# Kernel tuning notes

Measured on AMD Instinct MI355X. Metric: run time of the kernel, lower is better.

Reference implementation:

```python
import jax, jax.numpy as jnp
import numpy as np

B, T, V, E, U = 64, 128, 20000, 512, 1024


def _gru_dir(x_tbe, W, Uw, bi, bh):
    """Keras GRU (reset_after=True, gate order z,r,h). x_tbe: [T,B,E]."""
    # Precompute all input projections in one big GEMM: [T,B,3U]
    xg = jnp.einsum('tbe,eg->tbg', x_tbe, W) + bi

    def step(h, xg_t):
        hg = h @ Uw + bh                       # [B,3U]
        xz, xr, xh = jnp.split(xg_t, 3, axis=-1)
        hz, hr, hh = jnp.split(hg, 3, axis=-1)
        z = jax.nn.sigmoid(xz + hz)            # update gate
        r = jax.nn.sigmoid(xr + hr)            # reset gate
        hcand = jnp.tanh(xh + r * hh)          # reset_after=True form
        h_new = z * h + (1.0 - z) * hcand
        return h_new, h_new

    h0 = jnp.zeros((x_tbe.shape[1], Uw.shape[0]), x_tbe.dtype)
    hT, outs = jax.lax.scan(step, h0, xg)      # outs: [T,B,U]
    return outs, hT


def setup_inputs() -> dict:
    key = jax.random.key(0)
    ks = jax.random.split(key, 8)
    s_in = 1.0 / np.sqrt(E)
    s_rec = 1.0 / np.sqrt(U)
    return {
        'tokens': jax.random.randint(ks[0], (B, T), 0, V),
        'emb': jax.random.normal(ks[1], (V, E), jnp.float32) * 0.05,
        'Wf': jax.random.normal(ks[2], (E, 3 * U), jnp.float32) * s_in,
        'Uf': jax.random.normal(ks[3], (U, 3 * U), jnp.float32) * s_rec,
        'bif': jnp.zeros((3 * U,), jnp.float32),
        'bhf': jnp.zeros((3 * U,), jnp.float32),
        'Wb': jax.random.normal(ks[4], (E, 3 * U), jnp.float32) * s_in,
        'Ub': jax.random.normal(ks[5], (U, 3 * U), jnp.float32) * s_rec,
        'bib': jnp.zeros((3 * U,), jnp.float32),
        'bhb': jnp.zeros((3 * U,), jnp.float32),
    }


def reference(tokens, emb, Wf, Uf, bif, bhf, Wb, Ub, bib, bhb):
    tokens = tokens[:, ::-1]                    # tf.reverse(inputs, [-1])
    x = emb[tokens]                             # embedding lookup -> [B,T,E]
    x_t = jnp.swapaxes(x, 0, 1)                 # [T,B,E]
    out_f, h_f = _gru_dir(x_t, Wf, Uf, bif, bhf)
    out_b, h_b = _gru_dir(x_t[::-1], Wb, Ub, bib, bhb)
    out_b = out_b[::-1]                         # re-align backward outputs
    outputs = jnp.swapaxes(out_f + out_b, 0, 1)  # merge_mode='sum' -> [B,T,U]
    hidden = jnp.concatenate([h_f, h_b], axis=1)  # [B,2U]
    return outputs, hidden
```

## Files before the change

kernel.cpp:

```cpp
#include <hip/hip_runtime.h>
#include <hip/hip_bf16.h>

typedef float f32;
typedef __hip_bfloat16 bf16;
typedef unsigned int u32;
typedef unsigned short u16;

#define T_LEN 128
#define B_SZ  64
#define E_DIM 512
#define U_DIM 1024
#define G3    3072
#define BTU   (B_SZ * T_LEN * U_DIM)

typedef __attribute__((ext_vector_type(8))) __bf16 bf16x8;
typedef __attribute__((ext_vector_type(8))) u16  us8;
typedef __attribute__((ext_vector_type(4))) u16  us4;
typedef __attribute__((ext_vector_type(4))) f32  f32x4;

union F8 { us8 u; bf16x8 b; };

#define WS_USW 0u
#define WS_HQ  25165824u
#define WS_XG  26214400u

#define STEP_LDS 106496
#define XG_LDS   66048

__device__ __forceinline__ u32 f32_to_bf16_rne(f32 x) {
  u32 b = __float_as_uint(x);
  return (b + 0x7fffu + ((b >> 16) & 1u)) >> 16;
}

__global__ __launch_bounds__(256) void transpose_split(
    const f32* __restrict__ Uf, const f32* __restrict__ Ub, u16* __restrict__ USW)
{
  __shared__ f32 tile[32][33];
  const int d = blockIdx.z;
  const f32* Uw = d ? Ub : Uf;
  const int c0 = blockIdx.x * 32;
  const int k0 = blockIdx.y * 32;
  const int tx = threadIdx.x & 31;
  const int ty = threadIdx.x >> 5;
#pragma unroll
  for (int i = 0; i < 4; i++) {
    int kl = ty + i * 8;
    tile[kl][tx] = Uw[(size_t)(k0 + kl) * G3 + c0 + tx];
  }
  __syncthreads();
#pragma unroll
  for (int i = 0; i < 4; i++) {
    int cl = ty + i * 8;
    int c  = c0 + cl;
    f32 val = tile[tx][cl];
    int g = c >> 10, u = c & 1023;
    int blk = d * 128 + (u >> 3);
    int r   = g * 8 + (u & 7);
    u32 hib = f32_to_bf16_rne(val);
    f32 rem = val - __uint_as_float(hib << 16);
    u32 lob = f32_to_bf16_rne(rem);
    int k = k0 + tx;
    int slot = (k >> 3) ^ (r & 7);
    size_t base = ((size_t)blk * 2) * (24 * 1024);
    size_t off  = (size_t)r * 1024 + slot * 8 + (k & 7);
    USW[base + off] = (u16)hib;
    USW[base + (size_t)24 * 1024 + off] = (u16)lob;
  }
}

__global__ __launch_bounds__(256) void xg_gemm_mfma(
    const int* __restrict__ tokens, const f32* __restrict__ emb,
    const f32* __restrict__ Wf, const f32* __restrict__ bif,
    const f32* __restrict__ Wb, const f32* __restrict__ bib,
    bf16* __restrict__ XG)
{
  extern __shared__ u16 XL[];
  u16* Ash = XL;
  u16* Bsh = XL + 16384;
  int* tok_s = (int*)(XL + 32768);

  const int tid = threadIdx.x;
  const int n0 = blockIdx.x * 128;
  const int by = blockIdx.y;
  const int dir = by >> 6;
  const int s0 = (by & 63) * 2;
  const f32* W  = dir ? Wb : Wf;
  const f32* bi = dir ? bib : bif;

  if (tid < 128) {
    int srow = s0 + (tid >> 6);
    int b = tid & 63;
    int t_orig = dir ? srow : (T_LEN - 1 - srow);
    tok_s[tid] = tokens[b * T_LEN + t_orig];
  }
  __syncthreads();

  const int wv = tid >> 6;
  const int lane = tid & 63;
  const int arow = tid >> 1;
  const int akoff = (tid & 1) * 32;
  const int bcol = tid & 127;
  const int bkoff = (tid >> 7) * 32;

  f32x4 acc[2][8];
#pragma unroll
  for (int mi = 0; mi < 2; mi++)
#pragma unroll
    for (int ni = 0; ni < 8; ni++) acc[mi][ni] = (f32x4){0.f, 0.f, 0.f, 0.f};

  const f32* asrc0 = emb + (size_t)tok_s[arow] * E_DIM + akoff;

  for (int kk = 0; kk < 8; kk++) {
    __syncthreads();
    {
      const f32* src = asrc0 + kk * 64;
#pragma unroll
      for (int g = 0; g < 4; g++) {
        float4 v0 = *(const float4*)(src + g * 8);
        float4 v1 = *(const float4*)(src + g * 8 + 4);
        f32 vv[8] = {v0.x,v0.y,v0.z,v0.w,v1.x,v1.y,v1.z,v1.w};
        us8 h8, l8;
#pragma unroll
        for (int e = 0; e < 8; e++) {
          u32 bb = __float_as_uint(vv[e]);
          h8[e] = (u16)(bb >> 16);
          f32 rem = vv[e] - __uint_as_float(bb & 0xffff0000u);
          l8[e] = (u16)f32_to_bf16_rne(rem);
        }
        int sl = (((akoff >> 3) + g) ^ (arow & 7)) * 8;
        *(us8*)&Ash[(size_t)arow * 64 + sl] = h8;
        *(us8*)&Ash[(size_t)(128 + arow) * 64 + sl] = l8;
      }
    }
    {
      const f32* src = W + (size_t)(kk * 64 + bkoff) * G3 + n0 + bcol;
#pragma unroll
      for (int g = 0; g < 4; g++) {
        us8 h8, l8;
#pragma unroll
        for (int e = 0; e < 8; e++) {
          f32 v = src[(size_t)(g * 8 + e) * G3];
          u32 bb = __float_as_uint(v);
          h8[e] = (u16)(bb >> 16);
          f32 rem = v - __uint_as_float(bb & 0xffff0000u);
          l8[e] = (u16)f32_to_bf16_rne(rem);
        }
        int sl = (((bkoff >> 3) + g) ^ (bcol & 7)) * 8;
        *(us8*)&Bsh[(size_t)bcol * 64 + sl] = h8;
        *(us8*)&Bsh[(size_t)(128 + bcol) * 64 + sl] = l8;
      }
    }
    __syncthreads();
#pragma unroll
    for (int ks = 0; ks < 2; ks++) {
      F8 ah[2], al[2];
#pragma unroll
      for (int mi = 0; mi < 2; mi++) {
        int row = wv * 32 + mi * 16 + (lane & 15);
        int sl = ((ks * 4 + (lane >> 4)) ^ (row & 7)) * 8;
        ah[mi].u = *(const us8*)&Ash[(size_t)row * 64 + sl];
        al[mi].u = *(const us8*)&Ash[(size_t)(128 + row) * 64 + sl];
      }
#pragma unroll
      for (int ni = 0; ni < 8; ni++) {
        int col = ni * 16 + (lane & 15);
        int sl = ((ks * 4 + (lane >> 4)) ^ (col & 7)) * 8;
        F8 bh, bl;
        bh.u = *(const us8*)&Bsh[(size_t)col * 64 + sl];
        bl.u = *(const us8*)&Bsh[(size_t)(128 + col) * 64 + sl];
#pragma unroll
        for (int mi = 0; mi < 2; mi++) {
          acc[mi][ni] = __builtin_amdgcn_mfma_f32_16x16x32_bf16(ah[mi].b, bh.b, acc[mi][ni], 0, 0, 0);
          acc[mi][ni] = __builtin_amdgcn_mfma_f32_16x16x32_bf16(ah[mi].b, bl.b, acc[mi][ni], 0, 0, 0);
          acc[mi][ni] = __builtin_amdgcn_mfma_f32_16x16x32_bf16(al[mi].b, bh.b, acc[mi][ni], 0, 0, 0);
        }
      }
    }
  }
#pragma unroll
  for (int ni = 0; ni < 8; ni++) {
    int ncol = n0 + ni * 16 + (lane & 15);
    f32 bv = bi[ncol];
#pragma unroll
    for (int mi = 0; mi < 2; mi++) {
#pragma unroll
      for (int j = 0; j < 4; j++) {
        int row = wv * 32 + mi * 16 + (lane >> 4) * 4 + j;
        int srow = s0 + (row >> 6);
        int b = row & 63;
        XG[((size_t)(dir * T_LEN + srow) * B_SZ + b) * G3 + ncol] =
            __float2bfloat16(acc[mi][ni][j] + bv);
      }
    }
  }
}

__global__ __launch_bounds__(512) void gru_step4(
    const u16* __restrict__ USW,
    u16* __restrict__ Hq2,
    const u16* __restrict__ XG,
    const f32* __restrict__ bhf, const f32* __restrict__ bhb,
    f32* __restrict__ out, int s)
{
  extern __shared__ u16 Us[];
  const int blk = blockIdx.x;
  const int dir = blk >> 7;
  const int su  = (blk & 127) * 8;
  const int tid = threadIdx.x;
  const int lane = tid & 63;
  const int w  = tid >> 6;
  const int nw = w & 3, kw = w >> 2;

  const int bb = nw * 16 + (lane & 15);
  const int ko = (lane >> 4) * 8;
  const int kq = kw * 512;
  const int r0 = lane & 15;
  const int r1t = 16 + (lane & 15);
  const int r1 = r1t > 23 ? 23 : r1t;

  const int rb_h0 = (0 * 24 + r0) * 2048;
  const int rb_l0 = (1 * 24 + r0) * 2048;
  const int rb_h1 = (0 * 24 + r1) * 2048;
  const int rb_l1 = (1 * 24 + r1) * 2048;
  const int sw0 = r0 & 7, sw1 = r1 & 7;

  const int bufr = s & 1, bufw = bufr ^ 1;
  const u16* HrHi = Hq2 + (size_t)(((bufr * 2 + 0) * 2 + dir) * 64 + bb) * 1024;
  const u16* HrLo = Hq2 + (size_t)(((bufr * 2 + 1) * 2 + dir) * 64 + bb) * 1024;

  F8 h_hi0, h_lo0, h_hi1, h_lo1, h_hi2, h_lo2, h_hi3, h_lo3;
  if (s) {
    const u16* p = HrHi + kq + ko;
    const u16* q = HrLo + kq + ko;
    h_hi0.u = *(const us8*)(p);        h_lo0.u = *(const us8*)(q);
    h_hi1.u = *(const us8*)(p + 32);   h_lo1.u = *(const us8*)(q + 32);
    h_hi2.u = *(const us8*)(p + 64);   h_lo2.u = *(const us8*)(q + 64);
    h_hi3.u = *(const us8*)(p + 96);   h_lo3.u = *(const us8*)(q + 96);
  }

  {
    const us8* src = (const us8*)(USW + (size_t)blk * (2 * 24 * 1024));
    us8* dst = (us8*)Us;
#pragma unroll
    for (int i = 0; i < 12; i++) dst[tid + i * 512] = src[tid + i * 512];
  }

  __syncthreads();

  f32x4 acc0 = {0.f, 0.f, 0.f, 0.f};
  f32x4 acc1 = {0.f, 0.f, 0.f, 0.f};

#define DOMFMA(HHI, HLO, KS) { \
    const int slot = (kq >> 3) + (KS) * 4 + (lane >> 4); \
    F8 ah0, al0, ah1, al1; \
    ah0.u = *(const us8*)((const char*)Us + rb_h0 + ((slot ^ sw0) << 4)); \
    al0.u = *(const us8*)((const char*)Us + rb_l0 + ((slot ^ sw0) << 4)); \
    ah1.u = *(const us8*)((const char*)Us + rb_h1 + ((slot ^ sw1) << 4)); \
    al1.u = *(const us8*)((const char*)Us + rb_l1 + ((slot ^ sw1) << 4)); \
    acc0 = __builtin_amdgcn_mfma_f32_16x16x32_bf16(ah0.b, HHI.b, acc0, 0, 0, 0); \
    acc0 = __builtin_amdgcn_mfma_f32_16x16x32_bf16(ah0.b, HLO.b, acc0, 0, 0, 0); \
    acc0 = __builtin_amdgcn_mfma_f32_16x16x32_bf16(al0.b, HHI.b, acc0, 0, 0, 0); \
    acc1 = __builtin_amdgcn_mfma_f32_16x16x32_bf16(ah1.b, HHI.b, acc1, 0, 0, 0); \
    acc1 = __builtin_amdgcn_mfma_f32_16x16x32_bf16(ah1.b, HLO.b, acc1, 0, 0, 0); \
    acc1 = __builtin_amdgcn_mfma_f32_16x16x32_bf16(al1.b, HHI.b, acc1, 0, 0, 0); \
  }
#define LDH(HHI, HLO, KS) { \
    HHI.u = *(const us8*)(HrHi + kq + ko + (KS) * 32); \
    HLO.u = *(const us8*)(HrLo + kq + ko + (KS) * 32); \
  }

  if (s) {
    DOMFMA(h_hi0, h_lo0, 0)  LDH(h_hi0, h_lo0, 4)
    DOMFMA(h_hi1, h_lo1, 1)  LDH(h_hi1, h_lo1, 5)
    DOMFMA(h_hi2, h_lo2, 2)  LDH(h_hi2, h_lo2, 6)
    DOMFMA(h_hi3, h_lo3, 3)  LDH(h_hi3, h_lo3, 7)
    DOMFMA(h_hi0, h_lo0, 4)  LDH(h_hi0, h_lo0, 8)
    DOMFMA(h_hi1, h_lo1, 5)  LDH(h_hi1, h_lo1, 9)
    DOMFMA(h_hi2, h_lo2, 6)  LDH(h_hi2, h_lo2, 10)
    DOMFMA(h_hi3, h_lo3, 7)  LDH(h_hi3, h_lo3, 11)
    DOMFMA(h_hi0, h_lo0, 8)  LDH(h_hi0, h_lo0, 12)
    DOMFMA(h_hi1, h_lo1, 9)  LDH(h_hi1, h_lo1, 13)
    DOMFMA(h_hi2, h_lo2, 10) LDH(h_hi2, h_lo2, 14)
    DOMFMA(h_hi3, h_lo3, 11) LDH(h_hi3, h_lo3, 15)
    DOMFMA(h_hi0, h_lo0, 12)
    DOMFMA(h_hi1, h_lo1, 13)
    DOMFMA(h_hi2, h_lo2, 14)
    DOMFMA(h_hi3, h_lo3, 15)
  }
#undef DOMFMA
#undef LDH

  __syncthreads();
  f32* red = (f32*)(Us + 49152);
  if (kw == 1) {
    f32* p = red + (size_t)(nw * 64 + lane) * 8;
    *(f32x4*)p = acc0;
    *(f32x4*)(p + 4) = acc1;
  }
  __syncthreads();
  if (kw == 0) {
    const f32* p = red + (size_t)(nw * 64 + lane) * 8;
    f32x4 o0 = *(const f32x4*)p;
    f32x4 o1 = *(const f32x4*)(p + 4);
#pragma unroll
    for (int i = 0; i < 4; i++) { acc0[i] += o0[i]; acc1[i] += o1[i]; }

    f32 racc[4];
#pragma unroll
    for (int j = 0; j < 4; j++) racc[j] = __shfl_xor(acc0[j], 32);

    if (lane < 32) {
      const int ul0 = (lane >> 4) * 4;
      const int u0 = su + ul0;
      const u16* xgp = XG + ((size_t)(dir * T_LEN + s) * B_SZ + bb) * G3;
      us4 gz = *(const us4*)(xgp + u0 - su + su);
      gz = *(const us4*)(xgp + u0);
      us4 gr = *(const us4*)(xgp + 1024 + u0);
      us4 gh = *(const us4*)(xgp + 2048 + u0);
      us4 ohi = {0, 0, 0, 0}, olo = {0, 0, 0, 0};
      if (s) {
        ohi = *(const us4*)(HrHi + u0);
        olo = *(const us4*)(HrLo + u0);
      }
      const f32* bh = dir ? bhb : bhf;
      f32x4 hnv;
      us4 whi, wlo;
#pragma unroll
      for (int j = 0; j < 4; j++) {
        const int u = u0 + j;
        f32 hz = acc0[j] + bh[u];
        f32 hr = racc[j] + bh[1024 + u];
        f32 hh = acc1[j] + bh[2048 + u];
        f32 xz = __uint_as_float((u32)gz[j] << 16);
        f32 xr = __uint_as_float((u32)gr[j] << 16);
        f32 xh = __uint_as_float((u32)gh[j] << 16);
        f32 hold = __uint_as_float((u32)ohi[j] << 16) + __uint_as_float((u32)olo[j] << 16);

        f32 z  = 1.f / (1.f + expf(-(xz + hz)));
        f32 r  = 1.f / (1.f + expf(-(xr + hr)));
        f32 hc = tanhf(xh + r * hh);
        f32 hnew = z * hold + (1.f - z) * hc;

        u32 hib = f32_to_bf16_rne(hnew);
        f32 rem = hnew - __uint_as_float(hib << 16);
        u32 lob = f32_to_bf16_rne(rem);
        hnv[j] = hnew;
        whi[j] = (u16)hib;
        wlo[j] = (u16)lob;
      }
      u16* HwHi = Hq2 + (size_t)(((bufw * 2 + 0) * 2 + dir) * 64 + bb) * 1024;
      u16* HwLo = Hq2 + (size_t)(((bufw * 2 + 1) * 2 + dir) * 64 + bb) * 1024;
      *(us4*)(HwHi + u0) = whi;
      *(us4*)(HwLo + u0) = wlo;

      const int t = dir ? (T_LEN - 1 - s) : s;
      f32* op = out + ((size_t)bb * T_LEN + t) * U_DIM + u0;
      if (s < 64) {
        *(f32x4*)op = hnv;
      } else {
        f32x4 prev = *(const f32x4*)op;
#pragma unroll
        for (int j = 0; j < 4; j++) prev[j] += hnv[j];
        *(f32x4*)op = prev;
      }
      if (s == T_LEN - 1)
        *(f32x4*)(out + (size_t)BTU + (size_t)bb * 2048 + dir * 1024 + u0) = hnv;
    }
  }
}

extern "C" void kernel_launch(void* const* d_in, const int* in_sizes, int n_in,
                              void* d_out, int out_size, void* d_ws, size_t ws_size,
                              hipStream_t stream) {
  (void)in_sizes; (void)n_in; (void)out_size; (void)ws_size;
  const int* tokens = (const int*)d_in[0];
  const f32* emb = (const f32*)d_in[1];
  const f32* Wf  = (const f32*)d_in[2];
  const f32* Uf  = (const f32*)d_in[3];
  const f32* bif = (const f32*)d_in[4];
  const f32* bhf = (const f32*)d_in[5];
  const f32* Wb  = (const f32*)d_in[6];
  const f32* Ub  = (const f32*)d_in[7];
  const f32* bib = (const f32*)d_in[8];
  const f32* bhb = (const f32*)d_in[9];

  char* ws = (char*)d_ws;
  u16*  USW = (u16*)(ws + WS_USW);
  u16*  Hq2 = (u16*)(ws + WS_HQ);
  bf16* XG  = (bf16*)(ws + WS_XG);
  f32*  out = (f32*)d_out;

  transpose_split<<<dim3(96, 32, 2), 256, 0, stream>>>(Uf, Ub, USW);

  hipFuncSetAttribute((const void*)xg_gemm_mfma,
                      hipFuncAttributeMaxDynamicSharedMemorySize, XG_LDS);
  xg_gemm_mfma<<<dim3(24, 128), 256, XG_LDS, stream>>>(tokens, emb, Wf, bif, Wb, bib, XG);

  hipFuncSetAttribute((const void*)gru_step4,
                      hipFuncAttributeMaxDynamicSharedMemorySize, STEP_LDS);
  for (int s = 0; s < T_LEN; s++)
    gru_step4<<<256, 512, STEP_LDS, stream>>>(USW, Hq2, (const u16*)XG, bhf, bhb, out, s);
}
```

Baseline: 2.260 ms.

## Pack hidden-state hi/lo bf16 into u32 with unit-major layout, drop prefetch pipeline

New measurement: 1.892 ms. -16.3%, faster.

```diff
diff --git a/kernel.cpp b/kernel.cpp
--- a/kernel.cpp
+++ b/kernel.cpp
@@ -24,7 +24,7 @@
 #define WS_HQ  25165824u
 #define WS_XG  26214400u
 
-#define STEP_LDS 106496
+#define STEP_LDS 98304
 #define XG_LDS   66048
 
 __device__ __forceinline__ u32 f32_to_bf16_rne(f32 x) {
@@ -195,9 +195,9 @@
   }
 }
 
-__global__ __launch_bounds__(512) void gru_step4(
+__global__ __launch_bounds__(512) void gru_step5(
     const u16* __restrict__ USW,
-    u16* __restrict__ Hq2,
+    u32* __restrict__ Hq,
     const u16* __restrict__ XG,
     const f32* __restrict__ bhf, const f32* __restrict__ bhb,
     f32* __restrict__ out, int s)
@@ -211,9 +211,17 @@
   const int w  = tid >> 6;
   const int nw = w & 3, kw = w >> 2;
 
+  {
+    const us8* src = (const us8*)(USW + (size_t)blk * (2 * 24 * 1024));
+    us8* dst = (us8*)Us;
+    for (int i = tid; i < 6144; i += 512) dst[i] = src[i];
+  }
+
+  const u32* Hin  = Hq + (size_t)((s & 1) * 2 + dir) * (U_DIM * B_SZ);
+  u32*       Hout = Hq + (size_t)(((s + 1) & 1) * 2 + dir) * (U_DIM * B_SZ);
+
   const int bb = nw * 16 + (lane & 15);
   const int ko = (lane >> 4) * 8;
-  const int kq = kw * 512;
   const int r0 = lane & 15;
   const int r1t = 16 + (lane & 15);
   const int r1 = r1t > 23 ? 23 : r1t;
@@ -224,74 +232,42 @@
   const int rb_l1 = (1 * 24 + r1) * 2048;
   const int sw0 = r0 & 7, sw1 = r1 & 7;
 
-  const int bufr = s & 1, bufw = bufr ^ 1;
-  const u16* HrHi = Hq2 + (size_t)(((bufr * 2 + 0) * 2 + dir) * 64 + bb) * 1024;
-  const u16* HrLo = Hq2 + (size_t)(((bufr * 2 + 1) * 2 + dir) * 64 + bb) * 1024;
-
-  F8 h_hi0, h_lo0, h_hi1, h_lo1, h_hi2, h_lo2, h_hi3, h_lo3;
-  if (s) {
-    const u16* p = HrHi + kq + ko;
-    const u16* q = HrLo + kq + ko;
-    h_hi0.u = *(const us8*)(p);        h_lo0.u = *(const us8*)(q);
-    h_hi1.u = *(const us8*)(p + 32);   h_lo1.u = *(const us8*)(q + 32);
-    h_hi2.u = *(const us8*)(p + 64);   h_lo2.u = *(const us8*)(q + 64);
-    h_hi3.u = *(const us8*)(p + 96);   h_lo3.u = *(const us8*)(q + 96);
-  }
-
-  {
-    const us8* src = (const us8*)(USW + (size_t)blk * (2 * 24 * 1024));
-    us8* dst = (us8*)Us;
-#pragma unroll
-    for (int i = 0; i < 12; i++) dst[tid + i * 512] = src[tid + i * 512];
-  }
-
   __syncthreads();
 
   f32x4 acc0 = {0.f, 0.f, 0.f, 0.f};
   f32x4 acc1 = {0.f, 0.f, 0.f, 0.f};
 
-#define DOMFMA(HHI, HLO, KS) { \
-    const int slot = (kq >> 3) + (KS) * 4 + (lane >> 4); \
-    F8 ah0, al0, ah1, al1; \
-    ah0.u = *(const us8*)((const char*)Us + rb_h0 + ((slot ^ sw0) << 4)); \
-    al0.u = *(const us8*)((const char*)Us + rb_l0 + ((slot ^ sw0) << 4)); \
-    ah1.u = *(const us8*)((const char*)Us + rb_h1 + ((slot ^ sw1) << 4)); \
-    al1.u = *(const us8*)((const char*)Us + rb_l1 + ((slot ^ sw1) << 4)); \
-    acc0 = __builtin_amdgcn_mfma_f32_16x16x32_bf16(ah0.b, HHI.b, acc0, 0, 0, 0); \
-    acc0 = __builtin_amdgcn_mfma_f32_16x16x32_bf16(ah0.b, HLO.b, acc0, 0, 0, 0); \
-    acc0 = __builtin_amdgcn_mfma_f32_16x16x32_bf16(al0.b, HHI.b, acc0, 0, 0, 0); \
-    acc1 = __builtin_amdgcn_mfma_f32_16x16x32_bf16(ah1.b, HHI.b, acc1, 0, 0, 0); \
-    acc1 = __builtin_amdgcn_mfma_f32_16x16x32_bf16(ah1.b, HLO.b, acc1, 0, 0, 0); \
-    acc1 = __builtin_amdgcn_mfma_f32_16x16x32_bf16(al1.b, HHI.b, acc1, 0, 0, 0); \
-  }
-#define LDH(HHI, HLO, KS) { \
-    HHI.u = *(const us8*)(HrHi + kq + ko + (KS) * 32); \
-    HLO.u = *(const us8*)(HrLo + kq + ko + (KS) * 32); \
-  }
-
   if (s) {
-    DOMFMA(h_hi0, h_lo0, 0)  LDH(h_hi0, h_lo0, 4)
-    DOMFMA(h_hi1, h_lo1, 1)  LDH(h_hi1, h_lo1, 5)
-    DOMFMA(h_hi2, h_lo2, 2)  LDH(h_hi2, h_lo2, 6)
-    DOMFMA(h_hi3, h_lo3, 3)  LDH(h_hi3, h_lo3, 7)
-    DOMFMA(h_hi0, h_lo0, 4)  LDH(h_hi0, h_lo0, 8)
-    DOMFMA(h_hi1, h_lo1, 5)  LDH(h_hi1, h_lo1, 9)
-    DOMFMA(h_hi2, h_lo2, 6)  LDH(h_hi2, h_lo2, 10)
-    DOMFMA(h_hi3, h_lo3, 7)  LDH(h_hi3, h_lo3, 11)
-    DOMFMA(h_hi0, h_lo0, 8)  LDH(h_hi0, h_lo0, 12)
-    DOMFMA(h_hi1, h_lo1, 9)  LDH(h_hi1, h_lo1, 13)
-    DOMFMA(h_hi2, h_lo2, 10) LDH(h_hi2, h_lo2, 14)
-    DOMFMA(h_hi3, h_lo3, 11) LDH(h_hi3, h_lo3, 15)
-    DOMFMA(h_hi0, h_lo0, 12)
-    DOMFMA(h_hi1, h_lo1, 13)
-    DOMFMA(h_hi2, h_lo2, 14)
-    DOMFMA(h_hi3, h_lo3, 15)
-  }
-#undef DOMFMA
-#undef LDH
-
-  __syncthreads();
-  f32* red = (f32*)(Us + 49152);
+    for (int ks = 0; ks < 16; ks++) {
+      const int kb = kw * 512 + ks * 32;
+      const int slot = (kb >> 3) + (lane >> 4);
+      F8 ah0, al0, ah1, al1;
+      ah0.u = *(const us8*)((const char*)Us + rb_h0 + ((slot ^ sw0) << 4));
+      al0.u = *(const us8*)((const char*)Us + rb_l0 + ((slot ^ sw0) << 4));
+      ah1.u = *(const us8*)((const char*)Us + rb_h1 + ((slot ^ sw1) << 4));
+      al1.u = *(const us8*)((const char*)Us + rb_l1 + ((slot ^ sw1) << 4));
+
+      const int kbase = kb + ko;
+      u32 wd[8];
+#pragma unroll
+      for (int e = 0; e < 8; e++) wd[e] = Hin[(size_t)(kbase + e) * B_SZ + bb];
+      F8 bh_hi, bh_lo;
+#pragma unroll
+      for (int e = 0; e < 8; e++) {
+        bh_hi.u[e] = (u16)(wd[e] & 0xffffu);
+        bh_lo.u[e] = (u16)(wd[e] >> 16);
+      }
+      acc0 = __builtin_amdgcn_mfma_f32_16x16x32_bf16(ah0.b, bh_hi.b, acc0, 0, 0, 0);
+      acc0 = __builtin_amdgcn_mfma_f32_16x16x32_bf16(ah0.b, bh_lo.b, acc0, 0, 0, 0);
+      acc0 = __builtin_amdgcn_mfma_f32_16x16x32_bf16(al0.b, bh_hi.b, acc0, 0, 0, 0);
+      acc1 = __builtin_amdgcn_mfma_f32_16x16x32_bf16(ah1.b, bh_hi.b, acc1, 0, 0, 0);
+      acc1 = __builtin_amdgcn_mfma_f32_16x16x32_bf16(ah1.b, bh_lo.b, acc1, 0, 0, 0);
+      acc1 = __builtin_amdgcn_mfma_f32_16x16x32_bf16(al1.b, bh_hi.b, acc1, 0, 0, 0);
+    }
+  }
+
+  __syncthreads();
+  f32* red = (f32*)Us;
   if (kw == 1) {
     f32* p = red + (size_t)(nw * 64 + lane) * 8;
     *(f32x4*)p = acc0;
@@ -313,18 +289,11 @@
       const int ul0 = (lane >> 4) * 4;
       const int u0 = su + ul0;
       const u16* xgp = XG + ((size_t)(dir * T_LEN + s) * B_SZ + bb) * G3;
-      us4 gz = *(const us4*)(xgp + u0 - su + su);
-      gz = *(const us4*)(xgp + u0);
+      us4 gz = *(const us4*)(xgp + u0);
       us4 gr = *(const us4*)(xgp + 1024 + u0);
       us4 gh = *(const us4*)(xgp + 2048 + u0);
-      us4 ohi = {0, 0, 0, 0}, olo = {0, 0, 0, 0};
-      if (s) {
-        ohi = *(const us4*)(HrHi + u0);
-        olo = *(const us4*)(HrLo + u0);
-      }
       const f32* bh = dir ? bhb : bhf;
       f32x4 hnv;
-      us4 whi, wlo;
 #pragma unroll
       for (int j = 0; j < 4; j++) {
         const int u = u0 + j;
@@ -334,7 +303,9 @@
         f32 xz = __uint_as_float((u32)gz[j] << 16);
         f32 xr = __uint_as_float((u32)gr[j] << 16);
         f32 xh = __uint_as_float((u32)gh[j] << 16);
-        f32 hold = __uint_as_float((u32)ohi[j] << 16) + __uint_as_float((u32)olo[j] << 16);
+
+        u32 hw = s ? Hin[(size_t)u * B_SZ + bb] : 0u;
+        f32 hold = __uint_as_float(hw << 16) + __uint_as_float(hw & 0xffff0000u);
 
         f32 z  = 1.f / (1.f + expf(-(xz + hz)));
         f32 r  = 1.f / (1.f + expf(-(xr + hr)));
@@ -344,14 +315,9 @@
         u32 hib = f32_to_bf16_rne(hnew);
         f32 rem = hnew - __uint_as_float(hib << 16);
         u32 lob = f32_to_bf16_rne(rem);
+        Hout[(size_t)u * B_SZ + bb] = hib | (lob << 16);
         hnv[j] = hnew;
-        whi[j] = (u16)hib;
-        wlo[j] = (u16)lob;
-      }
-      u16* HwHi = Hq2 + (size_t)(((bufw * 2 + 0) * 2 + dir) * 64 + bb) * 1024;
-      u16* HwLo = Hq2 + (size_t)(((bufw * 2 + 1) * 2 + dir) * 64 + bb) * 1024;
-      *(us4*)(HwHi + u0) = whi;
-      *(us4*)(HwLo + u0) = wlo;
+      }
 
       const int t = dir ? (T_LEN - 1 - s) : s;
       f32* op = out + ((size_t)bb * T_LEN + t) * U_DIM + u0;
@@ -386,7 +352,7 @@
 
   char* ws = (char*)d_ws;
   u16*  USW = (u16*)(ws + WS_USW);
-  u16*  Hq2 = (u16*)(ws + WS_HQ);
+  u32*  Hq  = (u32*)(ws + WS_HQ);
   bf16* XG  = (bf16*)(ws + WS_XG);
   f32*  out = (f32*)d_out;
 
@@ -396,8 +362,8 @@
                       hipFuncAttributeMaxDynamicSharedMemorySize, XG_LDS);
   xg_gemm_mfma<<<dim3(24, 128), 256, XG_LDS, stream>>>(tokens, emb, Wf, bif, Wb, bib, XG);
 
-  hipFuncSetAttribute((const void*)gru_step4,
+  hipFuncSetAttribute((const void*)gru_step5,
                       hipFuncAttributeMaxDynamicSharedMemorySize, STEP_LDS);
   for (int s = 0; s < T_LEN; s++)
-    gru_step4<<<256, 512, STEP_LDS, stream>>>(USW, Hq2, (const u16*)XG, bhf, bhb, out, s);
-}
+    gru_step5<<<256, 512, STEP_LDS, stream>>>(USW, Hq, (const u16*)XG, bhf, bhb, out, s);
+}
```
